# Optimization experiments

Hardware: AMD Instinct MI355X
Metric: run time of the kernel (lower is better)

## Reference

```python
import jax, jax.numpy as jnp
import numpy as np

INF = 1000000000.0
D = 1024


def setup_inputs() -> dict:
    key = jax.random.key(0)
    k_enc, k_r = jax.random.split(key)
    encoding = jax.random.normal(k_enc, (8, 2048, D), dtype=jnp.float32)
    R = jax.random.normal(k_r, (D, D), dtype=jnp.float32) / D  # init_with_zeros=False
    return {"encoding": encoding, "R": R}


def reference(encoding, R):
    b, n, d = encoding.shape
    # Q = encoding @ R ; scores = Q @ encoding^T  (bilinear relation attention)
    encR = jnp.einsum("bnd,de->bne", encoding, R)          # [b, n, d]
    scores = jnp.einsum("bnd,bmd->bnm", encR, encoding)     # [b, n, n]
    # causal mask: -INF above the diagonal (use_mask=True)
    mask = jnp.where(jnp.tril(jnp.ones((n, n), dtype=bool)), 0.0, -INF).astype(scores.dtype)
    A = jax.nn.softmax(scores + mask, axis=2)               # [b, n, n]
    return jnp.einsum("bnm,bmd->bnd", A, encoding)          # [b, n, d]
```

## Files before the change

### kernel.cpp

```cpp
#include <hip/hip_runtime.h>
#include <hip/hip_bf16.h>


typedef __attribute__((ext_vector_type(4))) float f32x4;
typedef __attribute__((ext_vector_type(4))) unsigned u32x4;
typedef __attribute__((ext_vector_type(8))) __fp16 f16x8;
typedef __attribute__((ext_vector_type(4))) __fp16 f16x4;
typedef __attribute__((ext_vector_type(2))) __fp16 f16x2;

#define MFMA16H(A, B, C) __builtin_amdgcn_mfma_f32_16x16x32_f16(A, B, C, 0, 0, 0)

__device__ __forceinline__ f16x4 cvt4h(f32x4 a) {
    union { f16x4 v; f16x2 h[2]; } r;
    r.h[0] = __builtin_amdgcn_cvt_pkrtz(a[0], a[1]);
    r.h[1] = __builtin_amdgcn_cvt_pkrtz(a[2], a[3]);
    return r.v;
}

__device__ __forceinline__ void gload16(const void* g, void* l) {
    __builtin_amdgcn_global_load_lds(
        (const __attribute__((address_space(1))) unsigned*)g,
        (__attribute__((address_space(3))) unsigned*)l, 16, 0, 0);
}

#define BAR() do { __builtin_amdgcn_sched_barrier(0); \
                   __builtin_amdgcn_s_barrier();      \
                   __builtin_amdgcn_sched_barrier(0); } while (0)

__global__ __launch_bounds__(256) void transpose_cvt_kernel(
    const float* __restrict__ src, __fp16* __restrict__ dstT,
    __fp16* __restrict__ dstH, int R, int C)
{
    __shared__ __align__(16) char lt[64 * 128];
    const int t = threadIdx.x;
    const int bz = blockIdx.z;
    const int r0 = blockIdx.x * 64, c0 = blockIdx.y * 64;
    const size_t so = (size_t)bz * R * C;
    const int tr = t >> 4;
    const int tc4 = (t & 15) * 4;
#pragma unroll
    for (int p = 0; p < 4; ++p) {
        int rl = tr + 16 * p;
        f32x4 x = *(const f32x4*)(src + so + (size_t)(r0 + rl) * C + c0 + tc4);
        f16x4 h = cvt4h(x);
        if (dstH) *(f16x4*)(dstH + so + (size_t)(r0 + rl) * C + c0 + tc4) = h;
        *(f16x4*)(lt + rl * 128 + ((tc4 * 2) ^ ((rl & 7) << 4))) = h;
    }
    __syncthreads();
#pragma unroll
    for (int p = 0; p < 4; ++p) {
        int dl = tr + 16 * p;
#pragma unroll
        for (int j = 0; j < 4; ++j) {
            int kl = (t & 15) + 16 * j;
            __fp16 v = *(const __fp16*)(lt + kl * 128 + ((dl * 2) ^ ((kl & 7) << 4)));
            dstT[so + (size_t)(c0 + dl) * R + r0 + kl] = v;
        }
    }
}

__global__ __launch_bounds__(512, 2) void gemm_qr256(
    const __fp16* __restrict__ encH, const __fp16* __restrict__ Rt,
    __fp16* __restrict__ Qh)
{
    __shared__ __align__(16) char lds[131072];
    const int t = threadIdx.x;
    const int w = t >> 6, l = t & 63;
    const int l15 = l & 15, lg = (l >> 4) & 3;
    const int wr = w >> 2, wc = w & 3;
    const int bm = ((int)blockIdx.x >> 2) * 256;
    const int bn = ((int)blockIdx.x & 3) * 256;
    const __fp16* Ag = encH + (size_t)bm * 1024;
    const __fp16* Bg = Rt + (size_t)bn * 1024;

    const int srow = 32 * w + (l >> 2);
    const int slg = ((l & 3) - ((l >> 3) & 3)) & 3;
    const int slotr = ((l >> 4) + ((l & 15) >> 1)) & 3;

    f32x4 acc[8][4];
#pragma unroll
    for (int i = 0; i < 8; ++i)
#pragma unroll
        for (int j = 0; j < 4; ++j) acc[i][j] = (f32x4){0.f, 0.f, 0.f, 0.f};

    auto stage = [&](int op, int tile, int kh) {
        const __fp16* src = (op ? Bg : Ag) + (size_t)srow * 1024 + tile * 64 + kh * 32 + slg * 8;
        char* dst = lds + (tile & 1) * 65536 + op * 32768 + kh * 16384 + w * 2048;
        gload16(src, dst);
        gload16(src + (size_t)16 * 1024, dst + 1024);
    };
    auto rdA = [&](int buf, int ks, int mf) {
        return *(const f16x8*)(lds + buf * 65536 + ks * 16384
                               + (128 * wr + 16 * mf + l15) * 64 + slotr * 16);
    };
    auto rdB = [&](int buf, int ks, int nf) {
        return *(const f16x8*)(lds + buf * 65536 + 32768 + ks * 16384
                               + (64 * wc + 16 * nf + l15) * 64 + slotr * 16);
    };

    stage(0, 0, 0); stage(1, 0, 0); stage(0, 0, 1); stage(1, 0, 1);
    stage(0, 1, 0); stage(1, 1, 0);

    f16x8 afr[4], bfr[4];

#define MF16(mbase)                                                     \
    __builtin_amdgcn_s_setprio(1);                                      \
    _Pragma("unroll") for (int mf = 0; mf < 4; ++mf)                    \
        _Pragma("unroll") for (int nf = 0; nf < 4; ++nf)                \
            acc[(mbase) + mf][nf] = MFMA16H(afr[mf], bfr[nf], acc[(mbase) + mf][nf]); \
    __builtin_amdgcn_s_setprio(0);

    for (int i = 0; i < 8; ++i) {
        const bool lastI = (i == 7);
        asm volatile("s_waitcnt vmcnt(8)" ::: "memory");
        BAR();
#pragma unroll
        for (int nf = 0; nf < 4; ++nf) bfr[nf] = rdB(0, 0, nf);
#pragma unroll
        for (int mf = 0; mf < 4; ++mf) afr[mf] = rdA(0, 0, mf);
        stage(0, 2 * i + 1, 1);
        MF16(0)
        BAR();
#pragma unroll
        for (int mf = 0; mf < 4; ++mf) afr[mf] = rdA(0, 0, mf + 4);
        stage(1, 2 * i + 1, 1);
        MF16(4)
        asm volatile("s_waitcnt vmcnt(8)" ::: "memory");
        BAR();
#pragma unroll
        for (int nf = 0; nf < 4; ++nf) bfr[nf] = rdB(0, 1, nf);
#pragma unroll
        for (int mf = 0; mf < 4; ++mf) afr[mf] = rdA(0, 1, mf);
        if (!lastI) stage(0, 2 * i + 2, 0);
        MF16(0)
        BAR();
#pragma unroll
        for (int mf = 0; mf < 4; ++mf) afr[mf] = rdA(0, 1, mf + 4);
        if (!lastI) stage(1, 2 * i + 2, 0);
        MF16(4)
        if (!lastI) asm volatile("s_waitcnt vmcnt(8)" ::: "memory");
        else        asm volatile("s_waitcnt vmcnt(4)" ::: "memory");
        BAR();
#pragma unroll
        for (int nf = 0; nf < 4; ++nf) bfr[nf] = rdB(1, 0, nf);
#pragma unroll
        for (int mf = 0; mf < 4; ++mf) afr[mf] = rdA(1, 0, mf);
        if (!lastI) stage(0, 2 * i + 2, 1);
        MF16(0)
        BAR();
#pragma unroll
        for (int mf = 0; mf < 4; ++mf) afr[mf] = rdA(1, 0, mf + 4);
        if (!lastI) stage(1, 2 * i + 2, 1);
        MF16(4)
        if (!lastI) asm volatile("s_waitcnt vmcnt(8)" ::: "memory");
        else        asm volatile("s_waitcnt vmcnt(0)" ::: "memory");
        BAR();
#pragma unroll
        for (int nf = 0; nf < 4; ++nf) bfr[nf] = rdB(1, 1, nf);
#pragma unroll
        for (int mf = 0; mf < 4; ++mf) afr[mf] = rdA(1, 1, mf);
        if (!lastI) stage(0, 2 * i + 3, 0);
        MF16(0)
        BAR();
#pragma unroll
        for (int mf = 0; mf < 4; ++mf) afr[mf] = rdA(1, 1, mf + 4);
        if (!lastI) stage(1, 2 * i + 3, 0);
        MF16(4)
    }
#undef MF16

#pragma unroll
    for (int mf = 0; mf < 8; ++mf)
#pragma unroll
        for (int nf = 0; nf < 4; ++nf)
#pragma unroll
            for (int rg = 0; rg < 4; ++rg) {
                int rr = bm + 128 * wr + 16 * mf + 4 * lg + rg;
                int cc = bn + 64 * wc + 16 * nf + l15;
                Qh[(size_t)rr * 1024 + cc] = (__fp16)acc[mf][nf][rg];
            }
}

template <int CMODE>
__device__ __forceinline__ void gemm_core(
    const __fp16* __restrict__ A, const __fp16* __restrict__ B,
    char* __restrict__ Cptr, int ldA, int ldB, int ldC, int K, bool diag)
{
    __shared__ __align__(16) char sA[128 * 128];
    __shared__ __align__(16) char sB[128 * 128];
    const int t = threadIdx.x;
    const int w = t >> 6, l = t & 63;
    const int l15 = l & 15, lg = l >> 4;
    const int r0 = (w >> 1) * 64, c0 = (w & 1) * 64;
    const int swz = (l15 & 7) << 4;

    f32x4 acc[4][4];
#pragma unroll
    for (int i = 0; i < 4; ++i)
#pragma unroll
        for (int j = 0; j < 4; ++j) acc[i][j] = (f32x4){0.f, 0.f, 0.f, 0.f};

    const int strow = 32 * w + (l >> 3);
    const int gsrc = (((l & 7) ^ (l >> 3)) << 3);
    const __fp16* pa = A + (size_t)strow * ldA + gsrc;
    const __fp16* pb = B + (size_t)strow * ldB + gsrc;

    for (int kk = 0; kk < K; kk += 64) {
        __syncthreads();
#pragma unroll
        for (int i = 0; i < 4; ++i) {
            gload16(pa + (size_t)(8 * i) * ldA + kk, sA + w * 4096 + i * 1024);
            gload16(pb + (size_t)(8 * i) * ldB + kk, sB + w * 4096 + i * 1024);
        }
        __syncthreads();
#pragma unroll
        for (int ks = 0; ks < 2; ++ks) {
            f16x8 af[4], bf[4];
#pragma unroll
            for (int mt = 0; mt < 4; ++mt)
                af[mt] = *(const f16x8*)(sA + (r0 + 16 * mt + l15) * 128 + ((64 * ks + 16 * lg) ^ swz));
#pragma unroll
            for (int nt = 0; nt < 4; ++nt)
                bf[nt] = *(const f16x8*)(sB + (c0 + 16 * nt + l15) * 128 + ((64 * ks + 16 * lg) ^ swz));
#pragma unroll
            for (int mt = 0; mt < 4; ++mt)
#pragma unroll
                for (int nt = 0; nt < 4; ++nt)
                    acc[mt][nt] = MFMA16H(af[mt], bf[nt], acc[mt][nt]);
        }
    }
#pragma unroll
    for (int mt = 0; mt < 4; ++mt)
#pragma unroll
        for (int nt = 0; nt < 4; ++nt)
#pragma unroll
            for (int rg = 0; rg < 4; ++rg) {
                int rr = r0 + 16 * mt + 4 * lg + rg;
                int cc = c0 + 16 * nt + l15;
                float v = acc[mt][nt][rg];
                if (CMODE == 2) {
                    *(float*)(Cptr + ((size_t)rr * ldC + cc) * 4) = v;
                } else {
                    if (CMODE == 1 && diag && cc > rr) v = -30000.f;
                    *(__fp16*)(Cptr + ((size_t)rr * ldC + cc) * 2) = (__fp16)v;
                }
            }
}

__global__ __launch_bounds__(256) void gemm_s(
    const __fp16* __restrict__ Qh, const __fp16* __restrict__ encH,
    __fp16* __restrict__ S)
{
    const int b = (int)blockIdx.x & 7;
    int rem = 135 - ((int)blockIdx.x >> 3);
    int qt = 0;
    while (rem > qt) { rem -= qt + 1; ++qt; }
    const int kt = rem;
    const size_t bo = (size_t)b * 2048 * 1024;
    const size_t so = (size_t)b * 2048 * 2048;
    gemm_core<1>(Qh + bo + (size_t)(qt * 128) * 1024,
                 encH + bo + (size_t)(kt * 128) * 1024,
                 (char*)(S + so + (size_t)(qt * 128) * 2048 + kt * 128),
                 1024, 1024, 2048, 1024, qt == kt);
}

__global__ __launch_bounds__(256) void gemm_pv(
    const __fp16* __restrict__ P, const __fp16* __restrict__ encT,
    float* __restrict__ out)
{
    const int b = (int)blockIdx.x & 7;
    const int r = (int)blockIdx.x >> 3;
    const int qtb = 15 - (r >> 3);
    const int dblk = r & 7;
    const size_t so = (size_t)b * 2048 * 2048;
    const size_t to = (size_t)b * 1024 * 2048;
    const int K = 128 * (qtb + 1);
    gemm_core<2>(P + so + (size_t)(qtb * 128) * 2048,
                 encT + to + (size_t)(dblk * 128) * 2048,
                 (char*)(out + (size_t)b * 2048 * 1024 + (size_t)(qtb * 128) * 1024 + dblk * 128),
                 2048, 2048, 1024, K, false);
}

__global__ __launch_bounds__(256) void softmax_kernel(__fp16* __restrict__ S)
{
    const int t = threadIdx.x;
    const int wv = t >> 6, l = t & 63;
    const int r = blockIdx.x * 4 + wv;
    const int b = blockIdx.y;
    __fp16* row = S + ((size_t)b * 2048 + r) * 2048;
    const int L = ((r >> 7) + 1) << 7;

    float v[4][8];
    float mx = -1e30f;
#pragma unroll
    for (int i = 0; i < 4; ++i) {
        int c0 = 8 * l + 512 * i;
        if (c0 < L) {
            f16x8 h = *reinterpret_cast<const f16x8*>(row + c0);
#pragma unroll
            for (int j = 0; j < 8; ++j) { v[i][j] = (float)h[j]; mx = fmaxf(mx, v[i][j]); }
        } else {
#pragma unroll
            for (int j = 0; j < 8; ++j) v[i][j] = -1e30f;
        }
    }
#pragma unroll
    for (int off = 1; off < 64; off <<= 1) mx = fmaxf(mx, __shfl_xor(mx, off));
    float sm = 0.f;
#pragma unroll
    for (int i = 0; i < 4; ++i)
#pragma unroll
        for (int j = 0; j < 8; ++j) { v[i][j] = __expf(v[i][j] - mx); sm += v[i][j]; }
#pragma unroll
    for (int off = 1; off < 64; off <<= 1) sm += __shfl_xor(sm, off);
    const float inv = 1.f / sm;
#pragma unroll
    for (int i = 0; i < 4; ++i) {
        int c0 = 8 * l + 512 * i;
        if (c0 < L) {
            union { f16x8 v8; f16x2 h[4]; } o;
#pragma unroll
            for (int j = 0; j < 4; ++j)
                o.h[j] = __builtin_amdgcn_cvt_pkrtz(v[i][2 * j] * inv, v[i][2 * j + 1] * inv);
            *reinterpret_cast<f16x8*>(row + c0) = o.v8;
        }
    }
}

__global__ __launch_bounds__(256) void qr_gemm_kernel(
    const float* __restrict__ A, const float* __restrict__ B, float* C)
{
    __shared__ __align__(16) char sA[128 * 64];
    __shared__ __align__(16) char sB[128 * 64];
    const int t = threadIdx.x;
    const int w = t >> 6, l = t & 63;
    const int l15 = l & 15, lg = l >> 4;
    const int bm = blockIdx.x * 128;
    const int bn = blockIdx.y * 128;

    f32x4 acc[4][4];
#pragma unroll
    for (int i = 0; i < 4; ++i)
#pragma unroll
        for (int j = 0; j < 4; ++j) acc[i][j] = (f32x4){0.f, 0.f, 0.f, 0.f};

    const int kq = 4 * (t & 7);
    const int i2 = t >> 3;

    for (int kk = 0; kk < 1024; kk += 32) {
#pragma unroll
        for (int it = 0; it < 4; ++it) {
            int m = i2 + 32 * it;
            f32x4 x = *reinterpret_cast<const f32x4*>(&A[(size_t)(bm + m) * 1024 + kk + kq]);
            *reinterpret_cast<f16x4*>(sA + m * 64 + ((2 * kq) ^ (((m >> 1) & 3) << 4))) = cvt4h(x);
        }
        {
            int n0 = 4 * i2;
            f32x4 x[4];
#pragma unroll
            for (int r = 0; r < 4; ++r)
                x[r] = *reinterpret_cast<const f32x4*>(&B[(size_t)(kk + kq + r) * 1024 + bn + n0]);
#pragma unroll
            for (int j = 0; j < 4; ++j) {
                int n = n0 + j;
                union { f16x4 v; f16x2 h[2]; } s;
                s.h[0] = __builtin_amdgcn_cvt_pkrtz(x[0][j], x[1][j]);
                s.h[1] = __builtin_amdgcn_cvt_pkrtz(x[2][j], x[3][j]);
                *reinterpret_cast<f16x4*>(sB + n * 64 + ((2 * kq) ^ (((n >> 1) & 3) << 4))) = s.v;
            }
        }
        __syncthreads();
        f16x8 af[4], bfv[4];
        const int r0 = (w >> 1) * 64, c0 = (w & 1) * 64;
#pragma unroll
        for (int mt = 0; mt < 4; ++mt) {
            int m = r0 + 16 * mt + l15;
            af[mt] = *reinterpret_cast<f16x8*>(sA + m * 64 + ((16 * lg) ^ (((m >> 1) & 3) << 4)));
        }
#pragma unroll
        for (int nt = 0; nt < 4; ++nt) {
            int n = c0 + 16 * nt + l15;
            bfv[nt] = *reinterpret_cast<f16x8*>(sB + n * 64 + ((16 * lg) ^ (((n >> 1) & 3) << 4)));
        }
#pragma unroll
        for (int mt = 0; mt < 4; ++mt)
#pragma unroll
            for (int nt = 0; nt < 4; ++nt)
                acc[mt][nt] = MFMA16H(af[mt], bfv[nt], acc[mt][nt]);
        __syncthreads();
    }
#pragma unroll
    for (int mt = 0; mt < 4; ++mt)
#pragma unroll
        for (int nt = 0; nt < 4; ++nt)
#pragma unroll
            for (int rg = 0; rg < 4; ++rg) {
                int row = bm + (w >> 1) * 64 + 16 * mt + 4 * lg + rg;
                int col = bn + (w & 1) * 64 + 16 * nt + l15;
                C[(size_t)row * 1024 + col] = acc[mt][nt][rg];
            }
}

__global__ __launch_bounds__(256) void s_gemm_kernel(
    const float* __restrict__ Q, const float* __restrict__ enc, __fp16* __restrict__ S)
{
    __shared__ __align__(16) char sA[128 * 64];
    __shared__ __align__(16) char sB[128 * 64];
    const int t = threadIdx.x;
    const int w = t >> 6, l = t & 63;
    const int l15 = l & 15, lg = l >> 4;

    int rem = 135 - (int)blockIdx.x;
    int qt = 0;
    while (rem > qt) { rem -= qt + 1; ++qt; }
    const int kt = rem;
    const int b = blockIdx.y;
    const float* Arow = Q + ((size_t)b * 2048 + qt * 128) * 1024;
    const float* Brow = enc + ((size_t)b * 2048 + kt * 128) * 1024;

    f32x4 acc[4][4];
#pragma unroll
    for (int i = 0; i < 4; ++i)
#pragma unroll
        for (int j = 0; j < 4; ++j) acc[i][j] = (f32x4){0.f, 0.f, 0.f, 0.f};

    const int kq = 4 * (t & 7);
    const int i2 = t >> 3;

    for (int kk = 0; kk < 1024; kk += 32) {
#pragma unroll
        for (int it = 0; it < 4; ++it) {
            int m = i2 + 32 * it;
            int sw = (2 * kq) ^ (((m >> 1) & 3) << 4);
            f32x4 xa = *reinterpret_cast<const f32x4*>(&Arow[(size_t)m * 1024 + kk + kq]);
            f32x4 xb = *reinterpret_cast<const f32x4*>(&Brow[(size_t)m * 1024 + kk + kq]);
            *reinterpret_cast<f16x4*>(sA + m * 64 + sw) = cvt4h(xa);
            *reinterpret_cast<f16x4*>(sB + m * 64 + sw) = cvt4h(xb);
        }
        __syncthreads();
        f16x8 af[4], bfv[4];
        const int r0 = (w >> 1) * 64, c0 = (w & 1) * 64;
#pragma unroll
        for (int mt = 0; mt < 4; ++mt) {
            int m = r0 + 16 * mt + l15;
            af[mt] = *reinterpret_cast<f16x8*>(sA + m * 64 + ((16 * lg) ^ (((m >> 1) & 3) << 4)));
        }
#pragma unroll
        for (int nt = 0; nt < 4; ++nt) {
            int n = c0 + 16 * nt + l15;
            bfv[nt] = *reinterpret_cast<f16x8*>(sB + n * 64 + ((16 * lg) ^ (((n >> 1) & 3) << 4)));
        }
#pragma unroll
        for (int mt = 0; mt < 4; ++mt)
#pragma unroll
            for (int nt = 0; nt < 4; ++nt)
                acc[mt][nt] = MFMA16H(af[mt], bfv[nt], acc[mt][nt]);
        __syncthreads();
    }
    const int r0 = (w >> 1) * 64, c0 = (w & 1) * 64;
#pragma unroll
    for (int mt = 0; mt < 4; ++mt)
#pragma unroll
        for (int nt = 0; nt < 4; ++nt)
#pragma unroll
            for (int rg = 0; rg < 4; ++rg) {
                int rt = r0 + 16 * mt + 4 * lg + rg;
                int ct = c0 + 16 * nt + l15;
                float v = acc[mt][nt][rg];
                if (kt == qt && ct > rt) v = -30000.f;
                S[((size_t)b * 2048 + qt * 128 + rt) * 2048 + kt * 128 + ct] = (__fp16)v;
            }
}

__global__ __launch_bounds__(512) void pv_gemm_kernel(
    const __fp16* __restrict__ P, const float* __restrict__ enc, float* __restrict__ out)
{
    __shared__ __align__(16) char sA[128 * 128];
    __shared__ __align__(16) char sB[128 * 128];
    const int t = threadIdx.x;
    const int w = t >> 6, l = t & 63;
    const int l15 = l & 15, lg = (l >> 4) & 3;
    const int wq = w >> 2, wdv = w & 3;
    const int qtb = 15 - (int)blockIdx.x;
    const int dblk = blockIdx.y;
    const int b = blockIdx.z;
    const int q0 = 128 * qtb;
    const int nkv = 128 * (qtb + 1);
    const __fp16* Pbase = P + ((size_t)b * 2048 + q0) * 2048;
    const float* Eb = enc + (size_t)b * 2048 * 1024;

    f32x4 acc[4][2];
#pragma unroll
    for (int i = 0; i < 4; ++i)
#pragma unroll
        for (int j = 0; j < 2; ++j) acc[i][j] = (f32x4){0.f, 0.f, 0.f, 0.f};

    const int ar = t >> 2, aseg = t & 3;
    const int ba = t >> 5, bdq = t & 31;

    for (int kv0 = 0; kv0 < nkv; kv0 += 64) {
        __syncthreads();
        {
            const __fp16* src = Pbase + (size_t)ar * 2048 + kv0 + 16 * aseg;
            u32x4 v0 = *reinterpret_cast<const u32x4*>(src);
            u32x4 v1 = *reinterpret_cast<const u32x4*>(src + 8);
            const int sw = (ar & 7) << 4;
            *reinterpret_cast<u32x4*>(sA + ar * 128 + ((32 * aseg) ^ sw)) = v0;
            *reinterpret_cast<u32x4*>(sA + ar * 128 + ((32 * aseg + 16) ^ sw)) = v1;
        }
        {
            const float* src = Eb + (size_t)(kv0 + 4 * ba) * 1024 + 128 * dblk + 4 * bdq;
            f32x4 x0 = *reinterpret_cast<const f32x4*>(src);
            f32x4 x1 = *reinterpret_cast<const f32x4*>(src + 1024);
            f32x4 x2 = *reinterpret_cast<const f32x4*>(src + 2048);
            f32x4 x3 = *reinterpret_cast<const f32x4*>(src + 3072);
#pragma unroll
            for (int j = 0; j < 4; ++j) {
                int d = 4 * bdq + j;
                union { f16x4 v; f16x2 h[2]; } s;
                s.h[0] = __builtin_amdgcn_cvt_pkrtz(x0[j], x1[j]);
                s.h[1] = __builtin_amdgcn_cvt_pkrtz(x2[j], x3[j]);
                *reinterpret_cast<f16x4*>(sB + d * 128 + ((8 * ba) ^ ((d & 7) << 4))) = s.v;
            }
        }
        __syncthreads();
#pragma unroll
        for (int ks = 0; ks < 2; ++ks) {
            f16x8 afr[4], bfr[2];
#pragma unroll
            for (int mt = 0; mt < 4; ++mt) {
                int rr = 64 * wq + 16 * mt + l15;
                afr[mt] = *reinterpret_cast<f16x8*>(sA + rr * 128 + ((64 * ks + 16 * lg) ^ ((rr & 7) << 4)));
            }
#pragma unroll
            for (int nt = 0; nt < 2; ++nt) {
                int d = 32 * wdv + 16 * nt + l15;
                bfr[nt] = *reinterpret_cast<f16x8*>(sB + d * 128 + ((64 * ks + 16 * lg) ^ ((d & 7) << 4)));
            }
#pragma unroll
            for (int mt = 0; mt < 4; ++mt)
#pragma unroll
                for (int nt = 0; nt < 2; ++nt)
                    acc[mt][nt] = MFMA16H(afr[mt], bfr[nt], acc[mt][nt]);
        }
    }
#pragma unroll
    for (int mt = 0; mt < 4; ++mt)
#pragma unroll
        for (int nt = 0; nt < 2; ++nt)
#pragma unroll
            for (int rg = 0; rg < 4; ++rg) {
                size_t row = (size_t)b * 2048 + q0 + 64 * wq + 16 * mt + 4 * lg + rg;
                int col = 128 * dblk + 32 * wdv + 16 * nt + l15;
                out[row * 1024 + col] = acc[mt][nt][rg];
            }
}

extern "C" void kernel_launch(void* const* d_in, const int* in_sizes, int n_in,
                              void* d_out, int out_size, void* d_ws, size_t ws_size,
                              hipStream_t stream)
{
    const float* enc = (const float*)d_in[0];
    const float* R = (const float*)d_in[1];
    float* out = (float*)d_out;
    const size_t MB = 1u << 20;

    if (ws_size >= 98 * MB) {
        __fp16* S = (__fp16*)d_ws;
        __fp16* encT = (__fp16*)((char*)d_ws + 64 * MB);
        __fp16* Rt = (__fp16*)((char*)d_ws + 96 * MB);
        __fp16* Qh = (__fp16*)d_out;
        __fp16* encH = (__fp16*)d_out + (size_t)16384 * 1024;

        transpose_cvt_kernel<<<dim3(32, 16, 8), 256, 0, stream>>>(enc, encT, encH, 2048, 1024);
        transpose_cvt_kernel<<<dim3(16, 16, 1), 256, 0, stream>>>(R, Rt, (__fp16*)nullptr, 1024, 1024);
        gemm_qr256<<<dim3(256), 512, 0, stream>>>(encH, Rt, Qh);
        gemm_s<<<dim3(1088), 256, 0, stream>>>(Qh, encH, S);
        softmax_kernel<<<dim3(512, 8), 256, 0, stream>>>(S);
        gemm_pv<<<dim3(1024), 256, 0, stream>>>(S, encT, out);
    } else {
        __fp16* S = (__fp16*)d_ws;
        qr_gemm_kernel<<<dim3(128, 8), 256, 0, stream>>>(enc, R, out);
        s_gemm_kernel<<<dim3(136, 8), 256, 0, stream>>>(out, enc, S);
        softmax_kernel<<<dim3(512, 8), 256, 0, stream>>>(S);
        pv_gemm_kernel<<<dim3(16, 8, 8), 512, 0, stream>>>(S, enc, out);
    }
}
```

Measured before the change: 183.3 us.

## Replace S and PV GEMMs with 256x128 double-buffered pipelined tiles

Replaces the 128x128 single-buffered gemm_core with a 256x128-tile core using 512 threads, a 96KB double-buffered LDS ring, asynchronous global-to-LDS staging interleaved with MFMA phases, and setprio around MFMAs. The S kernel now tiles causally in 256-row query blocks with a per-element diagonal mask. The PV kernel pairs a short and a long causal row-block per workgroup to balance work. Softmax takes the mask granularity as a parameter (256 here), so more masked entries are computed and exponentiated, which adds some work.

```diff
diff --git a/kernel.cpp b/kernel.cpp
--- a/kernel.cpp
+++ b/kernel.cpp
@@ -182,17 +182,20 @@
 }
 
 template <int CMODE>
-__device__ __forceinline__ void gemm_core(
-    const __fp16* __restrict__ A, const __fp16* __restrict__ B,
-    char* __restrict__ Cptr, int ldA, int ldB, int ldC, int K, bool diag)
-{
-    __shared__ __align__(16) char sA[128 * 128];
-    __shared__ __align__(16) char sB[128 * 128];
+__device__ __forceinline__ void core256x128(
+    const __fp16* __restrict__ A, int ldA, const __fp16* __restrict__ B, int ldB,
+    char* __restrict__ Cptr, int ldC, int K, int rowOff, int colOff, bool maskDiag)
+{
+    __shared__ __align__(16) char lds[98304];
     const int t = threadIdx.x;
     const int w = t >> 6, l = t & 63;
-    const int l15 = l & 15, lg = l >> 4;
-    const int r0 = (w >> 1) * 64, c0 = (w & 1) * 64;
-    const int swz = (l15 & 7) << 4;
+    const int l15 = l & 15, lg = (l >> 4) & 3;
+    const int wr = w >> 1, wc = w & 1;
+
+    const int srowA = 32 * w + (l >> 2);
+    const int srowB = 16 * w + (l >> 2);
+    const int slg = ((l & 3) - ((l >> 3) & 3)) & 3;
+    const int slotr = ((l >> 4) + ((l & 15) >> 1)) & 3;
 
     f32x4 acc[4][4];
 #pragma unroll
@@ -200,95 +203,143 @@
 #pragma unroll
         for (int j = 0; j < 4; ++j) acc[i][j] = (f32x4){0.f, 0.f, 0.f, 0.f};
 
-    const int strow = 32 * w + (l >> 3);
-    const int gsrc = (((l & 7) ^ (l >> 3)) << 3);
-    const __fp16* pa = A + (size_t)strow * ldA + gsrc;
-    const __fp16* pb = B + (size_t)strow * ldB + gsrc;
-
-    for (int kk = 0; kk < K; kk += 64) {
-        __syncthreads();
-#pragma unroll
-        for (int i = 0; i < 4; ++i) {
-            gload16(pa + (size_t)(8 * i) * ldA + kk, sA + w * 4096 + i * 1024);
-            gload16(pb + (size_t)(8 * i) * ldB + kk, sB + w * 4096 + i * 1024);
-        }
-        __syncthreads();
-#pragma unroll
-        for (int ks = 0; ks < 2; ++ks) {
-            f16x8 af[4], bf[4];
-#pragma unroll
-            for (int mt = 0; mt < 4; ++mt)
-                af[mt] = *(const f16x8*)(sA + (r0 + 16 * mt + l15) * 128 + ((64 * ks + 16 * lg) ^ swz));
-#pragma unroll
-            for (int nt = 0; nt < 4; ++nt)
-                bf[nt] = *(const f16x8*)(sB + (c0 + 16 * nt + l15) * 128 + ((64 * ks + 16 * lg) ^ swz));
-#pragma unroll
-            for (int mt = 0; mt < 4; ++mt)
-#pragma unroll
-                for (int nt = 0; nt < 4; ++nt)
-                    acc[mt][nt] = MFMA16H(af[mt], bf[nt], acc[mt][nt]);
-        }
-    }
-#pragma unroll
-    for (int mt = 0; mt < 4; ++mt)
-#pragma unroll
-        for (int nt = 0; nt < 4; ++nt)
+    auto stageA = [&](int tile, int kh) {
+        const __fp16* src = A + (size_t)srowA * ldA + tile * 64 + kh * 32 + slg * 8;
+        char* dst = lds + (tile & 1) * 49152 + kh * 16384 + w * 2048;
+        gload16(src, dst);
+        gload16(src + (size_t)16 * ldA, dst + 1024);
+    };
+    auto stageB = [&](int tile, int kh) {
+        const __fp16* src = B + (size_t)srowB * ldB + tile * 64 + kh * 32 + slg * 8;
+        char* dst = lds + (tile & 1) * 49152 + 32768 + kh * 8192 + w * 1024;
+        gload16(src, dst);
+    };
+    auto rdA = [&](int buf, int kh, int mf) {
+        return *(const f16x8*)(lds + buf * 49152 + kh * 16384
+                               + (64 * wr + 16 * mf + l15) * 64 + slotr * 16);
+    };
+    auto rdB = [&](int buf, int kh, int nf) {
+        return *(const f16x8*)(lds + buf * 49152 + 32768 + kh * 8192
+                               + (64 * wc + 16 * nf + l15) * 64 + slotr * 16);
+    };
+
+    stageA(0, 0); stageB(0, 0);
+    stageA(0, 1); stageB(0, 1);
+    stageA(1, 0); stageB(1, 0);
+
+    f16x8 afr[4], bfr[4];
+    const int nIter = K >> 7;
+
+#define MFPH()                                                          \
+    __builtin_amdgcn_s_setprio(1);                                      \
+    _Pragma("unroll") for (int mf = 0; mf < 4; ++mf)                    \
+        _Pragma("unroll") for (int nf = 0; nf < 4; ++nf)                \
+            acc[mf][nf] = MFMA16H(afr[mf], bfr[nf], acc[mf][nf]);       \
+    __builtin_amdgcn_s_setprio(0);
+
+    for (int i = 0; i < nIter; ++i) {
+        const bool lastI = (i == nIter - 1);
+        asm volatile("s_waitcnt vmcnt(6)" ::: "memory");
+        BAR();
+#pragma unroll
+        for (int nf = 0; nf < 4; ++nf) bfr[nf] = rdB(0, 0, nf);
+#pragma unroll
+        for (int mf = 0; mf < 4; ++mf) afr[mf] = rdA(0, 0, mf);
+        stageA(2 * i + 1, 1); stageB(2 * i + 1, 1);
+        MFPH()
+        asm volatile("s_waitcnt vmcnt(6)" ::: "memory");
+        BAR();
+#pragma unroll
+        for (int nf = 0; nf < 4; ++nf) bfr[nf] = rdB(0, 1, nf);
+#pragma unroll
+        for (int mf = 0; mf < 4; ++mf) afr[mf] = rdA(0, 1, mf);
+        if (!lastI) { stageA(2 * i + 2, 0); stageB(2 * i + 2, 0); }
+        MFPH()
+        if (!lastI) asm volatile("s_waitcnt vmcnt(6)" ::: "memory");
+        else        asm volatile("s_waitcnt vmcnt(3)" ::: "memory");
+        BAR();
+#pragma unroll
+        for (int nf = 0; nf < 4; ++nf) bfr[nf] = rdB(1, 0, nf);
+#pragma unroll
+        for (int mf = 0; mf < 4; ++mf) afr[mf] = rdA(1, 0, mf);
+        if (!lastI) { stageA(2 * i + 2, 1); stageB(2 * i + 2, 1); }
+        MFPH()
+        if (!lastI) asm volatile("s_waitcnt vmcnt(6)" ::: "memory");
+        else        asm volatile("s_waitcnt vmcnt(0)" ::: "memory");
+        BAR();
+#pragma unroll
+        for (int nf = 0; nf < 4; ++nf) bfr[nf] = rdB(1, 1, nf);
+#pragma unroll
+        for (int mf = 0; mf < 4; ++mf) afr[mf] = rdA(1, 1, mf);
+        if (!lastI) { stageA(2 * i + 3, 0); stageB(2 * i + 3, 0); }
+        MFPH()
+    }
+#undef MFPH
+    BAR();
+
+#pragma unroll
+    for (int mf = 0; mf < 4; ++mf)
+#pragma unroll
+        for (int nf = 0; nf < 4; ++nf)
 #pragma unroll
             for (int rg = 0; rg < 4; ++rg) {
-                int rr = r0 + 16 * mt + 4 * lg + rg;
-                int cc = c0 + 16 * nt + l15;
-                float v = acc[mt][nt][rg];
+                int rr = 64 * wr + 16 * mf + 4 * lg + rg;
+                int cc = 64 * wc + 16 * nf + l15;
+                float v = acc[mf][nf][rg];
                 if (CMODE == 2) {
                     *(float*)(Cptr + ((size_t)rr * ldC + cc) * 4) = v;
                 } else {
-                    if (CMODE == 1 && diag && cc > rr) v = -30000.f;
+                    if (maskDiag && colOff + cc > rowOff + rr) v = -30000.f;
                     *(__fp16*)(Cptr + ((size_t)rr * ldC + cc) * 2) = (__fp16)v;
                 }
             }
 }
 
-__global__ __launch_bounds__(256) void gemm_s(
+__global__ __launch_bounds__(512, 2) void gemm_s256(
     const __fp16* __restrict__ Qh, const __fp16* __restrict__ encH,
     __fp16* __restrict__ S)
 {
     const int b = (int)blockIdx.x & 7;
-    int rem = 135 - ((int)blockIdx.x >> 3);
+    const int r = (int)blockIdx.x >> 3;
     int qt = 0;
-    while (rem > qt) { rem -= qt + 1; ++qt; }
-    const int kt = rem;
+    while (r >= (qt + 1) * (qt + 2)) ++qt;
+    const int nt = r - qt * (qt + 1);
     const size_t bo = (size_t)b * 2048 * 1024;
     const size_t so = (size_t)b * 2048 * 2048;
-    gemm_core<1>(Qh + bo + (size_t)(qt * 128) * 1024,
-                 encH + bo + (size_t)(kt * 128) * 1024,
-                 (char*)(S + so + (size_t)(qt * 128) * 2048 + kt * 128),
-                 1024, 1024, 2048, 1024, qt == kt);
-}
-
-__global__ __launch_bounds__(256) void gemm_pv(
+    core256x128<1>(Qh + bo + (size_t)(256 * qt) * 1024, 1024,
+                   encH + bo + (size_t)(128 * nt) * 1024, 1024,
+                   (char*)(S + so + (size_t)(256 * qt) * 2048 + 128 * nt), 2048,
+                   1024, 256 * qt, 128 * nt, (nt >> 1) == qt);
+}
+
+__global__ __launch_bounds__(512, 2) void gemm_pv256(
     const __fp16* __restrict__ P, const __fp16* __restrict__ encT,
     float* __restrict__ out)
 {
     const int b = (int)blockIdx.x & 7;
     const int r = (int)blockIdx.x >> 3;
-    const int qtb = 15 - (r >> 3);
-    const int dblk = r & 7;
+    const int a = r >> 3, dblk = r & 7;
     const size_t so = (size_t)b * 2048 * 2048;
     const size_t to = (size_t)b * 1024 * 2048;
-    const int K = 128 * (qtb + 1);
-    gemm_core<2>(P + so + (size_t)(qtb * 128) * 2048,
-                 encT + to + (size_t)(dblk * 128) * 2048,
-                 (char*)(out + (size_t)b * 2048 * 1024 + (size_t)(qtb * 128) * 1024 + dblk * 128),
-                 2048, 2048, 1024, K, false);
-}
-
-__global__ __launch_bounds__(256) void softmax_kernel(__fp16* __restrict__ S)
+    const size_t oo = (size_t)b * 2048 * 1024;
+#pragma unroll
+    for (int pass = 0; pass < 2; ++pass) {
+        const int qtb = pass ? 7 - a : a;
+        core256x128<2>(P + so + (size_t)(256 * qtb) * 2048, 2048,
+                       encT + to + (size_t)(128 * dblk) * 2048, 2048,
+                       (char*)(out + oo + (size_t)(256 * qtb) * 1024 + 128 * dblk), 1024,
+                       256 * (qtb + 1), 0, 0, false);
+    }
+}
+
+__global__ __launch_bounds__(256) void softmax_kernel(__fp16* __restrict__ S, int sh)
 {
     const int t = threadIdx.x;
     const int wv = t >> 6, l = t & 63;
     const int r = blockIdx.x * 4 + wv;
     const int b = blockIdx.y;
     __fp16* row = S + ((size_t)b * 2048 + r) * 2048;
-    const int L = ((r >> 7) + 1) << 7;
+    const int L = ((r >> sh) + 1) << sh;
 
     float v[4][8];
     float mx = -1e30f;
@@ -575,14 +626,14 @@
         transpose_cvt_kernel<<<dim3(32, 16, 8), 256, 0, stream>>>(enc, encT, encH, 2048, 1024);
         transpose_cvt_kernel<<<dim3(16, 16, 1), 256, 0, stream>>>(R, Rt, (__fp16*)nullptr, 1024, 1024);
         gemm_qr256<<<dim3(256), 512, 0, stream>>>(encH, Rt, Qh);
-        gemm_s<<<dim3(1088), 256, 0, stream>>>(Qh, encH, S);
-        softmax_kernel<<<dim3(512, 8), 256, 0, stream>>>(S);
-        gemm_pv<<<dim3(1024), 256, 0, stream>>>(S, encT, out);
+        gemm_s256<<<dim3(576), 512, 0, stream>>>(Qh, encH, S);
+        softmax_kernel<<<dim3(512, 8), 256, 0, stream>>>(S, 8);
+        gemm_pv256<<<dim3(256), 512, 0, stream>>>(S, encT, out);
     } else {
         __fp16* S = (__fp16*)d_ws;
         qr_gemm_kernel<<<dim3(128, 8), 256, 0, stream>>>(enc, R, out);
         s_gemm_kernel<<<dim3(136, 8), 256, 0, stream>>>(out, enc, S);
-        softmax_kernel<<<dim3(512, 8), 256, 0, stream>>>(S);
+        softmax_kernel<<<dim3(512, 8), 256, 0, stream>>>(S, 7);
         pv_gemm_kernel<<<dim3(16, 8, 8), 512, 0, stream>>>(S, enc, out);
     }
 }
```

Measured after the change: 177.8 us. -3.0%, faster.
